# Optimization experiments

Measured on AMD Instinct MI355X. Metric: run time of the kernel, lower is better.

## Reference

```python
import jax, jax.numpy as jnp
import numpy as np

N_NODES = 100000
N_EDGES = 1280000
D_IN = 64
D_HID = 64


def _sage_conv(x, src, dst, deg, Wl, bl, Wr):
    # gather source-node features per edge, scatter-mean to destination nodes
    msg = x[src]                                            # [E, d]
    agg = jax.ops.segment_sum(msg, dst, num_segments=N_NODES)  # [N, d]
    mean = agg / deg                                        # [N, d]
    # PyG SAGEConv: lin_l(aggregated) + lin_r(root); bias lives in lin_l
    return mean @ Wl.T + bl + x @ Wr.T


def setup_inputs() -> dict:
    key = jax.random.key(0)
    ks = jax.random.split(key, 10)
    x = jax.random.normal(ks[0], (N_NODES, D_IN), dtype=jnp.float32)
    edge_index = jax.random.randint(ks[1], (2, N_EDGES), 0, N_NODES, dtype=jnp.int64)
    s = 1.0 / np.sqrt(D_IN)
    W1l = jax.random.uniform(ks[2], (D_HID, D_IN), jnp.float32, -s, s)
    W1r = jax.random.uniform(ks[3], (D_HID, D_IN), jnp.float32, -s, s)
    b1 = jax.random.uniform(ks[4], (D_HID,), jnp.float32, -s, s)
    s2 = 1.0 / np.sqrt(D_HID)
    W2l = jax.random.uniform(ks[5], (D_HID, D_HID), jnp.float32, -s2, s2)
    W2r = jax.random.uniform(ks[6], (D_HID, D_HID), jnp.float32, -s2, s2)
    b2 = jax.random.uniform(ks[7], (D_HID,), jnp.float32, -s2, s2)
    Wh = jax.random.uniform(ks[8], (1, D_HID), jnp.float32, -s2, s2)
    bh = jax.random.uniform(ks[9], (1,), jnp.float32, -s2, s2)
    return {"x": x, "edge_index": edge_index, "W1l": W1l, "W1r": W1r, "b1": b1,
            "W2l": W2l, "W2r": W2r, "b2": b2, "Wh": Wh, "bh": bh}


def reference(x, edge_index, W1l, W1r, b1, W2l, W2r, b2, Wh, bh):
    src, dst = edge_index[0], edge_index[1]
    # in-degree for mean aggregation (clamped to avoid div-by-zero)
    deg = jax.ops.segment_sum(jnp.ones((N_EDGES,), jnp.float32), dst,
                              num_segments=N_NODES)
    deg = jnp.maximum(deg, 1.0)[:, None]                    # [N, 1]
    h = jax.nn.relu(_sage_conv(x, src, dst, deg, W1l, b1, W1r))
    h = jax.nn.relu(_sage_conv(h, src, dst, deg, W2l, b2, W2r))
    out = (h @ Wh.T + bh)[:, 0]                             # [N]
    return out, h
```

## Files before the change

### kernel.cpp

```cpp
#include <hip/hip_runtime.h>

#define N_NODES 100000
#define N_EDGES 1280000
#define D 64
#define NPAD 102400
#define CAP 48
#define NBUCK 391
#define AB 313
#define CVB 1024
#define NT32 3125
#define XQ (N_NODES * 16)

typedef __attribute__((ext_vector_type(8))) short bf16x8;
typedef __attribute__((ext_vector_type(4))) float f32x4;
typedef __attribute__((ext_vector_type(2))) float f32x2;

__device__ __forceinline__ unsigned short f2bf(float f) {
    union { float f; unsigned u; } c; c.f = f;
    unsigned u = c.u;
    return (unsigned short)((u + 0x7FFF + ((u >> 16) & 1)) >> 16);
}
__device__ __forceinline__ float fp8d(unsigned b) {
    unsigned t = ((b & 0x80u) << 24) | ((b & 0x7fu) << 20);
    union { unsigned u; float f; } c; c.u = t;
    return c.f * 1.32922799578491587e36f;
}
__device__ __forceinline__ unsigned char f2fp8(float f) {
    f = fminf(fmaxf(f, -448.f), 448.f);
    float g = f * 7.52316384526264005e-37f;
    union { float f; unsigned u; } c; c.f = g;
    unsigned gb = c.u;
    unsigned r = (((gb & 0x7fffffffu) + 0x7ffffu + ((gb >> 20) & 1u)) >> 20) & 0x7fu;
    return (unsigned char)(((gb >> 24) & 0x80u) | r);
}

__global__ __launch_bounds__(512) void prep_kernel(
    const float* __restrict__ x,
    const int* __restrict__ src, const int* __restrict__ dst,
    const float* __restrict__ W1l, const float* __restrict__ W1r,
    const float* __restrict__ W2l, const float* __restrict__ W2r,
    unsigned short* __restrict__ xb, unsigned short* __restrict__ h1b,
    unsigned char* __restrict__ x8, unsigned char* __restrict__ h8,
    unsigned short* __restrict__ wb,
    int* __restrict__ sorted, int* __restrict__ exclT)
{
    __shared__ int cntA[392];
    __shared__ int excl[392];
    __shared__ int stage_pk[4096];

    const int t   = threadIdx.x;
    const int bid = blockIdx.x;

    if (bid < AB) {
        const int e0 = bid * 4096;
        const int cbatch = min(4096, N_EDGES - e0);

        if (t < 392) cntA[t] = 0;
        __syncthreads();

        int mb[8], mr[8], mpk[8];
#pragma unroll
        for (int i = 0; i < 8; ++i) {
            int idx = i * 512 + t;
            mb[i] = -1;
            if (idx < cbatch) {
                int e = e0 + idx;
                int s = src[e], d = dst[e];
                int b = d >> 8;
                mb[i]  = b;
                mpk[i] = (s << 8) | (d & 255);
                mr[i]  = atomicAdd(&cntA[b], 1);
            }
        }
        __syncthreads();

        if (t < 64) {
            int pre[7], tot = 0;
            if (t < 56) {
#pragma unroll
                for (int i = 0; i < 7; ++i) { pre[i] = tot; tot += cntA[t * 7 + i]; }
            }
            int sc = tot;
#pragma unroll
            for (int off = 1; off < 64; off <<= 1) {
                int u = __shfl_up(sc, off, 64);
                if (t >= off) sc += u;
            }
            int ex = sc - tot;
            if (t < 56) {
#pragma unroll
                for (int i = 0; i < 7; ++i) excl[t * 7 + i] = ex + pre[i];
            }
        }
        __syncthreads();

#pragma unroll
        for (int i = 0; i < 8; ++i) {
            if (mb[i] >= 0)
                stage_pk[excl[mb[i]] + mr[i]] = mpk[i];
        }
        __syncthreads();

#pragma unroll
        for (int i = 0; i < 8; ++i) {
            int idx = i * 512 + t;
            if (idx < cbatch) sorted[e0 + idx] = stage_pk[idx];
        }
        if (t < 392) exclT[bid * 392 + t] = excl[t];
    } else {
        const int gtid = (bid - AB) * 512 + t;
        const int gsz  = CVB * 512;
        const int TOT  = XQ + 32 + 4096;
        for (int i = gtid; i < TOT; i += gsz) {
            if (i < XQ) {
                float4 v = ((const float4*)x)[i];
                ((ushort4*)xb)[i] = make_ushort4(f2bf(v.x), f2bf(v.y), f2bf(v.z), f2bf(v.w));
                ((uchar4*)x8)[i]  = make_uchar4(f2fp8(v.x), f2fp8(v.y), f2fp8(v.z), f2fp8(v.w));
            } else if (i < XQ + 32) {
                int k = i - XQ;
                if (k < 16) {
                    ((ushort4*)xb)[(size_t)N_NODES * 16 + k] = make_ushort4(0,0,0,0);
                    ((unsigned*)x8)[(size_t)N_NODES * 16 + k] = 0u;
                } else {
                    ((ushort4*)h1b)[(size_t)N_NODES * 16 + (k - 16)] = make_ushort4(0,0,0,0);
                    ((unsigned*)h8)[(size_t)N_NODES * 16 + (k - 16)] = 0u;
                }
            } else {
                int wf = i - XQ - 32;
                int m = wf >> 10, k = wf & 1023;
                const float* s = (m == 0) ? W1l : (m == 1) ? W1r : (m == 2) ? W2l : W2r;
                float4 v = ((const float4*)s)[k];
                ((ushort4*)wb)[m * 1024 + k] =
                    make_ushort4(f2bf(v.x), f2bf(v.y), f2bf(v.z), f2bf(v.w));
            }
        }
    }
}

__global__ __launch_bounds__(512) void binB_kernel(const int* __restrict__ sorted,
                                                   const int* __restrict__ exclT,
                                                   int* __restrict__ csr,
                                                   int* __restrict__ deg) {
    __shared__ int cur[256];
    __shared__ __align__(16) int lcsr[256 * CAP];

    const int t = threadIdx.x;
    const int k = blockIdx.x;

    if (t < 256) cur[t] = 0;
    __syncthreads();

    if (t < AB) {
        int s0  = exclT[t * 392 + k];
        int cnt = exclT[t * 392 + k + 1] - s0;
        const int* sp = sorted + t * 4096 + s0;
        if (cnt > 0) {
            int pk = sp[0];
            for (int e = 0; e < cnt; ++e) {
                int nxt = (e + 1 < cnt) ? sp[e + 1] : 0;
                int nl = pk & 255;
                int r  = atomicAdd(&cur[nl], 1);
                if (r < CAP) lcsr[nl * CAP + r] = pk >> 8;
                pk = nxt;
            }
        }
    }
    __syncthreads();

    const int base = k * 256;
    for (int i = t; i < 4096; i += 512) {
        int r = i >> 4, cc = i & 15;
        if (cc < 12) {
            int lenr = min(cur[r], CAP);
            if (cc * 4 < lenr)
                *(int4*)(csr + (size_t)(base + r) * CAP + cc * 4) =
                    *(const int4*)(lcsr + r * CAP + cc * 4);
        }
    }
    if (t < 256) deg[base + t] = cur[t];
}

template <int LAYER>
__global__ __launch_bounds__(512) void layer_kernel(
    const int* __restrict__ csr, const int* __restrict__ deg_g,
    const unsigned char*  __restrict__ feat8,
    const unsigned short* __restrict__ root_b,
    const unsigned short* __restrict__ wl_b,
    const float* __restrict__ bl,
    const unsigned short* __restrict__ wr_b,
    unsigned short* __restrict__ hout_b,
    unsigned char*  __restrict__ hout8,
    float* __restrict__ hout_f,
    const float* __restrict__ Wh, const float* __restrict__ bh,
    float* __restrict__ out)
{
    __shared__ __align__(16) char lds[10240];
    unsigned short* sA = (unsigned short*)lds;
    unsigned short* sX = sA + 32 * 72;
    float* sH    = (float*)lds;
    float* spart = (float*)(lds + 9216);

    const int tid = threadIdx.x;
    const int n0  = blockIdx.x * 32;

    {
        int row = tid >> 4, c4 = tid & 15;
        ushort4 x4 = ((const ushort4*)root_b)[(n0 + row) * 16 + c4];
        *(ushort4*)(sX + row * 72 + c4 * 4) = x4;
    }

    {
        const uint2* fb2 = (const uint2*)feat8;
        const int g   = tid >> 4;
        const int l   = tid & 15;
        const int h   = l >> 3;
        const int lo  = l & 7;
        const int n   = n0 + g;
        const int* rp = csr + (size_t)n * CAP;
        const int dg  = deg_g[n];
        const int id0 = rp[l];
        const int len = (dg < CAP) ? dg : CAP;
        f32x2 a0 = {0.f, 0.f}, a1 = {0.f, 0.f}, a2 = {0.f, 0.f}, a3 = {0.f, 0.f};

#if __has_builtin(__builtin_amdgcn_cvt_pk_f32_fp8)
#define GCHUNK(IDEXPR)                                                       \
        {                                                                    \
            int id_ = (IDEXPR);                                              \
            uint2 w[8];                                                      \
            _Pragma("unroll")                                                \
            for (int i = 0; i < 8; ++i)                                      \
                w[i] = fb2[(__shfl(id_, 2 * i + h, 16) << 3) + lo];          \
            _Pragma("unroll")                                                \
            for (int i = 0; i < 8; ++i) {                                    \
                a0 += __builtin_amdgcn_cvt_pk_f32_fp8((int)w[i].x, false);   \
                a1 += __builtin_amdgcn_cvt_pk_f32_fp8((int)w[i].x, true);    \
                a2 += __builtin_amdgcn_cvt_pk_f32_fp8((int)w[i].y, false);   \
                a3 += __builtin_amdgcn_cvt_pk_f32_fp8((int)w[i].y, true);    \
            }                                                                \
        }
#else
#define GCHUNK(IDEXPR)                                                       \
        {                                                                    \
            int id_ = (IDEXPR);                                              \
            uint2 w[8];                                                      \
            _Pragma("unroll")                                                \
            for (int i = 0; i < 8; ++i)                                      \
                w[i] = fb2[(__shfl(id_, 2 * i + h, 16) << 3) + lo];          \
            _Pragma("unroll")                                                \
            for (int i = 0; i < 8; ++i) {                                    \
                f32x2 p0 = {fp8d(w[i].x & 255), fp8d((w[i].x >> 8) & 255)};  \
                f32x2 p1 = {fp8d((w[i].x >> 16) & 255), fp8d(w[i].x >> 24)}; \
                f32x2 p2 = {fp8d(w[i].y & 255), fp8d((w[i].y >> 8) & 255)};  \
                f32x2 p3 = {fp8d((w[i].y >> 16) & 255), fp8d(w[i].y >> 24)}; \
                a0 += p0; a1 += p1; a2 += p2; a3 += p3;                      \
            }                                                                \
        }
#endif

        GCHUNK((l < len) ? id0 : N_NODES);
        for (int cb = 16; cb < len; cb += 16) {
            int idxl = cb + l;
            GCHUNK((idxl < len) ? rp[idxl] : N_NODES);
        }
#undef GCHUNK

        a0.x += __shfl_xor(a0.x, 8); a0.y += __shfl_xor(a0.y, 8);
        a1.x += __shfl_xor(a1.x, 8); a1.y += __shfl_xor(a1.y, 8);
        a2.x += __shfl_xor(a2.x, 8); a2.y += __shfl_xor(a2.y, 8);
        a3.x += __shfl_xor(a3.x, 8); a3.y += __shfl_xor(a3.y, 8);
        float inv = 1.0f / fmaxf((float)dg, 1.0f);
        if (h == 0) {
            *(ushort4*)(sA + g * 72 + lo * 8) =
                make_ushort4(f2bf(a0.x * inv), f2bf(a0.y * inv),
                             f2bf(a1.x * inv), f2bf(a1.y * inv));
            *(ushort4*)(sA + g * 72 + lo * 8 + 4) =
                make_ushort4(f2bf(a2.x * inv), f2bf(a2.y * inv),
                             f2bf(a3.x * inv), f2bf(a3.y * inv));
        }
    }
    __syncthreads();

    const int w8 = tid >> 6;
    const int rt = w8 & 1, jt = w8 >> 1;
    const int l64 = tid & 63;
    const int rowl = l64 & 15, quad = l64 >> 4;

    const unsigned short* ap = sA + (rt * 16 + rowl) * 72 + quad * 8;
    const unsigned short* xp = sX + (rt * 16 + rowl) * 72 + quad * 8;
    bf16x8 am0 = *(const bf16x8*)(ap);
    bf16x8 am1 = *(const bf16x8*)(ap + 32);
    bf16x8 ax0 = *(const bf16x8*)(xp);
    bf16x8 ax1 = *(const bf16x8*)(xp + 32);
    __syncthreads();

    const unsigned short* wlp = wl_b + (jt * 16 + rowl) * 64 + quad * 8;
    const unsigned short* wrp = wr_b + (jt * 16 + rowl) * 64 + quad * 8;
    bf16x8 b0 = *(const bf16x8*)(wlp);
    bf16x8 b1 = *(const bf16x8*)(wlp + 32);
    bf16x8 b2 = *(const bf16x8*)(wrp);
    bf16x8 b3 = *(const bf16x8*)(wrp + 32);
    f32x4 acc = {0.f, 0.f, 0.f, 0.f};
    acc = __builtin_amdgcn_mfma_f32_16x16x32_bf16(am0, b0, acc, 0, 0, 0);
    acc = __builtin_amdgcn_mfma_f32_16x16x32_bf16(am1, b1, acc, 0, 0, 0);
    acc = __builtin_amdgcn_mfma_f32_16x16x32_bf16(ax0, b2, acc, 0, 0, 0);
    acc = __builtin_amdgcn_mfma_f32_16x16x32_bf16(ax1, b3, acc, 0, 0, 0);
    float bj = bl[jt * 16 + rowl];

#pragma unroll
    for (int r = 0; r < 4; ++r) {
        int node = rt * 16 + quad * 4 + r;
        sH[node * 68 + jt * 16 + rowl] = fmaxf(acc[r] + bj, 0.f);
    }
    __syncthreads();

    if (LAYER == 2 && tid < 256) {
        int node = tid >> 3, q = tid & 7;
        float p = 0.f;
#pragma unroll
        for (int c = 0; c < 2; ++c) {
            float4 hv = *(const float4*)(sH + node * 68 + q * 8 + c * 4);
            float4 wv = ((const float4*)Wh)[q * 2 + c];
            p += hv.x * wv.x + hv.y * wv.y + hv.z * wv.z + hv.w * wv.w;
        }
        spart[tid] = p;
    }

    {
        int row = tid >> 4, c4 = tid & 15;
        int n = n0 + row;
        const float* hp = sH + row * 68 + c4 * 4;
        if (LAYER == 1) {
            ((ushort4*)hout_b)[n * 16 + c4] =
                make_ushort4(f2bf(hp[0]), f2bf(hp[1]), f2bf(hp[2]), f2bf(hp[3]));
            ((uchar4*)hout8)[n * 16 + c4] =
                make_uchar4(f2fp8(hp[0]), f2fp8(hp[1]), f2fp8(hp[2]), f2fp8(hp[3]));
        } else {
            ((float4*)hout_f)[n * 16 + c4] =
                make_float4(hp[0], hp[1], hp[2], hp[3]);
        }
    }

    if (LAYER == 2) {
        __syncthreads();
        if (tid < 32) {
            float s = bh[0];
#pragma unroll
            for (int q = 0; q < 8; ++q) s += spart[tid * 8 + q];
            out[n0 + tid] = s;
        }
    }
}

extern "C" void kernel_launch(void* const* d_in, const int* in_sizes, int n_in,
                              void* d_out, int out_size, void* d_ws, size_t ws_size,
                              hipStream_t stream) {
    const float* x   = (const float*)d_in[0];
    const int*   ei  = (const int*)d_in[1];
    const int*   src = ei;
    const int*   dst = ei + N_EDGES;
    const float* W1l = (const float*)d_in[2];
    const float* W1r = (const float*)d_in[3];
    const float* b1  = (const float*)d_in[4];
    const float* W2l = (const float*)d_in[5];
    const float* W2r = (const float*)d_in[6];
    const float* b2  = (const float*)d_in[7];
    const float* Wh  = (const float*)d_in[8];
    const float* bh  = (const float*)d_in[9];

    float* out   = (float*)d_out;
    float* h_out = out + N_NODES;

    int* wsi = (int*)d_ws;
    int* deg = wsi;
    int* csr = deg + NPAD;
    unsigned short* wb  = (unsigned short*)(csr + NBUCK * 256 * CAP);
    unsigned short* x_b = wb + 16384;
    unsigned short* h1b = x_b + (size_t)(N_NODES + 1) * D;
    unsigned char*  x8  = (unsigned char*)(h1b + (size_t)(N_NODES + 1) * D);
    unsigned char*  h8  = x8 + (size_t)(N_NODES + 1) * D;
    int* sorted = (int*)h1b;
    int* exclT  = sorted + AB * 4096;

    unsigned short* w1l_b = wb;
    unsigned short* w1r_b = wb + 4096;
    unsigned short* w2l_b = wb + 8192;
    unsigned short* w2r_b = wb + 12288;

    prep_kernel<<<AB + CVB, 512, 0, stream>>>(
        x, src, dst, W1l, W1r, W2l, W2r, x_b, h1b, x8, h8, wb, sorted, exclT);

    binB_kernel<<<NBUCK, 512, 0, stream>>>(sorted, exclT, csr, deg);

    layer_kernel<1><<<NT32, 512, 0, stream>>>(
        csr, deg, x8, x_b, w1l_b, b1, w1r_b, h1b, h8, nullptr,
        nullptr, nullptr, nullptr);
    layer_kernel<2><<<NT32, 512, 0, stream>>>(
        csr, deg, h8, h1b, w2l_b, b2, w2r_b, nullptr, nullptr, h_out,
        Wh, bh, out);
}
```

Measured before the change: 178.9 us.

## Split feature conversion across prep and binning kernels, halve per-thread bin segments

Part of the x/weight bf16/fp8 conversion moves from the prep kernel into extra blocks of the binning kernel, so it overlaps with the latency-bound bucket scatter, which otherwise leaves the GPU underused. The binning loop now splits each segment across two threads to shorten the serial atomic chain per thread. Weight and bias loads in the layer kernel are hoisted before the gather so their latency overlaps it. The cost is more register pressure in the layer kernel and a fixed split point that must be tuned.

```diff
diff --git a/kernel.cpp b/kernel.cpp
--- a/kernel.cpp
+++ b/kernel.cpp
@@ -7,9 +7,12 @@
 #define CAP 48
 #define NBUCK 391
 #define AB 313
-#define CVB 1024
 #define NT32 3125
 #define XQ (N_NODES * 16)
+#define CVTOT (XQ + 32 + 4096)
+#define SPLIT 720000
+#define CV1 384
+#define CV2 384
 
 typedef __attribute__((ext_vector_type(8))) short bf16x8;
 typedef __attribute__((ext_vector_type(4))) float f32x4;
@@ -32,6 +35,40 @@
     unsigned gb = c.u;
     unsigned r = (((gb & 0x7fffffffu) + 0x7ffffu + ((gb >> 20) & 1u)) >> 20) & 0x7fu;
     return (unsigned char)(((gb >> 24) & 0x80u) | r);
+}
+
+__device__ __forceinline__ void cvt_range(
+    int gtid, int gsz, int lo0, int hi,
+    const float* __restrict__ x,
+    const float* __restrict__ W1l, const float* __restrict__ W1r,
+    const float* __restrict__ W2l, const float* __restrict__ W2r,
+    unsigned short* __restrict__ xb, unsigned short* __restrict__ h1b,
+    unsigned char* __restrict__ x8, unsigned char* __restrict__ h8,
+    unsigned short* __restrict__ wb)
+{
+    for (int i = lo0 + gtid; i < hi; i += gsz) {
+        if (i < XQ) {
+            float4 v = ((const float4*)x)[i];
+            ((ushort4*)xb)[i] = make_ushort4(f2bf(v.x), f2bf(v.y), f2bf(v.z), f2bf(v.w));
+            ((uchar4*)x8)[i]  = make_uchar4(f2fp8(v.x), f2fp8(v.y), f2fp8(v.z), f2fp8(v.w));
+        } else if (i < XQ + 32) {
+            int k = i - XQ;
+            if (k < 16) {
+                ((ushort4*)xb)[(size_t)N_NODES * 16 + k] = make_ushort4(0,0,0,0);
+                ((unsigned*)x8)[(size_t)N_NODES * 16 + k] = 0u;
+            } else {
+                ((ushort4*)h1b)[(size_t)N_NODES * 16 + (k - 16)] = make_ushort4(0,0,0,0);
+                ((unsigned*)h8)[(size_t)N_NODES * 16 + (k - 16)] = 0u;
+            }
+        } else {
+            int wf = i - XQ - 32;
+            int m = wf >> 10, k = wf & 1023;
+            const float* s = (m == 0) ? W1l : (m == 1) ? W1r : (m == 2) ? W2l : W2r;
+            float4 v = ((const float4*)s)[k];
+            ((ushort4*)wb)[m * 1024 + k] =
+                make_ushort4(f2bf(v.x), f2bf(v.y), f2bf(v.z), f2bf(v.w));
+        }
+    }
 }
 
 __global__ __launch_bounds__(512) void prep_kernel(
@@ -109,75 +146,68 @@
         if (t < 392) exclT[bid * 392 + t] = excl[t];
     } else {
         const int gtid = (bid - AB) * 512 + t;
-        const int gsz  = CVB * 512;
-        const int TOT  = XQ + 32 + 4096;
-        for (int i = gtid; i < TOT; i += gsz) {
-            if (i < XQ) {
-                float4 v = ((const float4*)x)[i];
-                ((ushort4*)xb)[i] = make_ushort4(f2bf(v.x), f2bf(v.y), f2bf(v.z), f2bf(v.w));
-                ((uchar4*)x8)[i]  = make_uchar4(f2fp8(v.x), f2fp8(v.y), f2fp8(v.z), f2fp8(v.w));
-            } else if (i < XQ + 32) {
-                int k = i - XQ;
-                if (k < 16) {
-                    ((ushort4*)xb)[(size_t)N_NODES * 16 + k] = make_ushort4(0,0,0,0);
-                    ((unsigned*)x8)[(size_t)N_NODES * 16 + k] = 0u;
-                } else {
-                    ((ushort4*)h1b)[(size_t)N_NODES * 16 + (k - 16)] = make_ushort4(0,0,0,0);
-                    ((unsigned*)h8)[(size_t)N_NODES * 16 + (k - 16)] = 0u;
-                }
-            } else {
-                int wf = i - XQ - 32;
-                int m = wf >> 10, k = wf & 1023;
-                const float* s = (m == 0) ? W1l : (m == 1) ? W1r : (m == 2) ? W2l : W2r;
-                float4 v = ((const float4*)s)[k];
-                ((ushort4*)wb)[m * 1024 + k] =
-                    make_ushort4(f2bf(v.x), f2bf(v.y), f2bf(v.z), f2bf(v.w));
-            }
-        }
-    }
-}
-
-__global__ __launch_bounds__(512) void binB_kernel(const int* __restrict__ sorted,
-                                                   const int* __restrict__ exclT,
-                                                   int* __restrict__ csr,
-                                                   int* __restrict__ deg) {
+        cvt_range(gtid, CV1 * 512, 0, SPLIT,
+                  x, W1l, W1r, W2l, W2r, xb, h1b, x8, h8, wb);
+    }
+}
+
+__global__ __launch_bounds__(512) void binB_kernel(
+    const int* __restrict__ sorted, const int* __restrict__ exclT,
+    int* __restrict__ csr, int* __restrict__ deg,
+    const float* __restrict__ x,
+    const float* __restrict__ W1l, const float* __restrict__ W1r,
+    const float* __restrict__ W2l, const float* __restrict__ W2r,
+    unsigned short* __restrict__ xb, unsigned short* __restrict__ h1b,
+    unsigned char* __restrict__ x8, unsigned char* __restrict__ h8,
+    unsigned short* __restrict__ wb)
+{
     __shared__ int cur[256];
     __shared__ __align__(16) int lcsr[256 * CAP];
 
     const int t = threadIdx.x;
     const int k = blockIdx.x;
 
-    if (t < 256) cur[t] = 0;
-    __syncthreads();
-
-    if (t < AB) {
-        int s0  = exclT[t * 392 + k];
-        int cnt = exclT[t * 392 + k + 1] - s0;
-        const int* sp = sorted + t * 4096 + s0;
-        if (cnt > 0) {
-            int pk = sp[0];
-            for (int e = 0; e < cnt; ++e) {
-                int nxt = (e + 1 < cnt) ? sp[e + 1] : 0;
-                int nl = pk & 255;
-                int r  = atomicAdd(&cur[nl], 1);
-                if (r < CAP) lcsr[nl * CAP + r] = pk >> 8;
-                pk = nxt;
-            }
-        }
-    }
-    __syncthreads();
-
-    const int base = k * 256;
-    for (int i = t; i < 4096; i += 512) {
-        int r = i >> 4, cc = i & 15;
-        if (cc < 12) {
-            int lenr = min(cur[r], CAP);
-            if (cc * 4 < lenr)
-                *(int4*)(csr + (size_t)(base + r) * CAP + cc * 4) =
-                    *(const int4*)(lcsr + r * CAP + cc * 4);
-        }
-    }
-    if (t < 256) deg[base + t] = cur[t];
+    if (k < NBUCK) {
+        if (t < 256) cur[t] = 0;
+        __syncthreads();
+
+        for (int u = t; u < 2 * AB; u += 512) {
+            int seg = u >> 1, half = u & 1;
+            int s0  = exclT[seg * 392 + k];
+            int cnt = exclT[seg * 392 + k + 1] - s0;
+            int b0 = half ? (cnt >> 1) : 0;
+            int b1 = half ? cnt : (cnt >> 1);
+            const int* sp = sorted + seg * 4096 + s0 + b0;
+            int m = b1 - b0;
+            if (m > 0) {
+                int pk = sp[0];
+                for (int e = 0; e < m; ++e) {
+                    int nxt = (e + 1 < m) ? sp[e + 1] : 0;
+                    int nl = pk & 255;
+                    int r  = atomicAdd(&cur[nl], 1);
+                    if (r < CAP) lcsr[nl * CAP + r] = pk >> 8;
+                    pk = nxt;
+                }
+            }
+        }
+        __syncthreads();
+
+        const int base = k * 256;
+        for (int i = t; i < 4096; i += 512) {
+            int r = i >> 4, cc = i & 15;
+            if (cc < 12) {
+                int lenr = min(cur[r], CAP);
+                if (cc * 4 < lenr)
+                    *(int4*)(csr + (size_t)(base + r) * CAP + cc * 4) =
+                        *(const int4*)(lcsr + r * CAP + cc * 4);
+            }
+        }
+        if (t < 256) deg[base + t] = cur[t];
+    } else {
+        const int gtid = (k - NBUCK) * 512 + t;
+        cvt_range(gtid, CV2 * 512, SPLIT, CVTOT,
+                  x, W1l, W1r, W2l, W2r, xb, h1b, x8, h8, wb);
+    }
 }
 
 template <int LAYER>
@@ -203,6 +233,18 @@
     const int tid = threadIdx.x;
     const int n0  = blockIdx.x * 32;
 
+    const int w8 = tid >> 6;
+    const int rt = w8 & 1, jt = w8 >> 1;
+    const int l64 = tid & 63;
+    const int rowl = l64 & 15, quad = l64 >> 4;
+    const unsigned short* wlp = wl_b + (jt * 16 + rowl) * 64 + quad * 8;
+    const unsigned short* wrp = wr_b + (jt * 16 + rowl) * 64 + quad * 8;
+    bf16x8 b0 = *(const bf16x8*)(wlp);
+    bf16x8 b1 = *(const bf16x8*)(wlp + 32);
+    bf16x8 b2 = *(const bf16x8*)(wrp);
+    bf16x8 b3 = *(const bf16x8*)(wrp + 32);
+    float bj = bl[jt * 16 + rowl];
+
     {
         int row = tid >> 4, c4 = tid & 15;
         ushort4 x4 = ((const ushort4*)root_b)[(n0 + row) * 16 + c4];
@@ -280,11 +322,6 @@
     }
     __syncthreads();
 
-    const int w8 = tid >> 6;
-    const int rt = w8 & 1, jt = w8 >> 1;
-    const int l64 = tid & 63;
-    const int rowl = l64 & 15, quad = l64 >> 4;
-
     const unsigned short* ap = sA + (rt * 16 + rowl) * 72 + quad * 8;
     const unsigned short* xp = sX + (rt * 16 + rowl) * 72 + quad * 8;
     bf16x8 am0 = *(const bf16x8*)(ap);
@@ -293,18 +330,11 @@
     bf16x8 ax1 = *(const bf16x8*)(xp + 32);
     __syncthreads();
 
-    const unsigned short* wlp = wl_b + (jt * 16 + rowl) * 64 + quad * 8;
-    const unsigned short* wrp = wr_b + (jt * 16 + rowl) * 64 + quad * 8;
-    bf16x8 b0 = *(const bf16x8*)(wlp);
-    bf16x8 b1 = *(const bf16x8*)(wlp + 32);
-    bf16x8 b2 = *(const bf16x8*)(wrp);
-    bf16x8 b3 = *(const bf16x8*)(wrp + 32);
     f32x4 acc = {0.f, 0.f, 0.f, 0.f};
     acc = __builtin_amdgcn_mfma_f32_16x16x32_bf16(am0, b0, acc, 0, 0, 0);
     acc = __builtin_amdgcn_mfma_f32_16x16x32_bf16(am1, b1, acc, 0, 0, 0);
     acc = __builtin_amdgcn_mfma_f32_16x16x32_bf16(ax0, b2, acc, 0, 0, 0);
     acc = __builtin_amdgcn_mfma_f32_16x16x32_bf16(ax1, b3, acc, 0, 0, 0);
-    float bj = bl[jt * 16 + rowl];
 
 #pragma unroll
     for (int r = 0; r < 4; ++r) {
@@ -386,10 +416,12 @@
     unsigned short* w2l_b = wb + 8192;
     unsigned short* w2r_b = wb + 12288;
 
-    prep_kernel<<<AB + CVB, 512, 0, stream>>>(
+    prep_kernel<<<AB + CV1, 512, 0, stream>>>(
         x, src, dst, W1l, W1r, W2l, W2r, x_b, h1b, x8, h8, wb, sorted, exclT);
 
-    binB_kernel<<<NBUCK, 512, 0, stream>>>(sorted, exclT, csr, deg);
+    binB_kernel<<<NBUCK + CV2, 512, 0, stream>>>(
+        sorted, exclT, csr, deg,
+        x, W1l, W1r, W2l, W2r, x_b, h1b, x8, h8, wb);
 
     layer_kernel<1><<<NT32, 512, 0, stream>>>(
         csr, deg, x8, x_b, w1l_b, b1, w1r_b, h1b, h8, nullptr,
```

Result: faster. 174.1 us (-2.7%).
